# Optimization experiments

Measured on AMD Instinct MI355X. Metric: run time of the kernel, lower is better.

## Reference

```python
import jax, jax.numpy as jnp
import numpy as np

N, E = 100000, 1600000
IN, H, Z, C = 64, 128, 64, 2


def _glorot(key, fan_in, fan_out):
    s = jnp.sqrt(2.0 / (fan_in + fan_out)).astype(jnp.float32)
    return jax.random.normal(key, (fan_in, fan_out), dtype=jnp.float32) * s


def setup_inputs() -> dict:
    key = jax.random.key(0)
    ks = jax.random.split(key, 16)
    dims = [(IN, H), (H, H), (H, Z), (H, H), (H, Z), (Z, H), (H, H), (H, IN * C)]
    names = ['in', 'mu0', 'mu', 'si0', 'si', 'z', 'd0', 'out']
    inp = {
        'x': jax.random.normal(ks[0], (N, IN), dtype=jnp.float32),
        'eps': jax.random.normal(ks[1], (N, Z), dtype=jnp.float32),
        'edge_index': jax.random.randint(ks[2], (2, E), 0, N, dtype=jnp.int64),
    }
    for i, (nm, (fi, fo)) in enumerate(zip(names, dims)):
        inp[f'w_{nm}'] = _glorot(ks[3 + i], fi, fo)
        inp[f'b_{nm}'] = jnp.zeros((fo,), dtype=jnp.float32)
    return inp


def _gcn(x, W, b, src, dst, dinv):
    # PyG GCNConv: symmetric normalization with self-loops.
    h = x @ W                                      # [N, d_out]
    norm = (dinv[src] * dinv[dst])[:, None]        # [E, 1]
    agg = jax.ops.segment_sum(h[src] * norm, dst, num_segments=N)
    agg = agg + h * (dinv * dinv)[:, None]         # self-loop term (norm = 1/deg)
    return agg + b


def reference(x, edge_index, eps,
              w_in, b_in, w_mu0, b_mu0, w_mu, b_mu,
              w_si0, b_si0, w_si, b_si,
              w_z, b_z, w_d0, b_d0, w_out, b_out):
    src, dst = edge_index[0], edge_index[1]
    deg = jax.ops.segment_sum(jnp.ones((E,), jnp.float32), dst, num_segments=N) + 1.0
    dinv = jax.lax.rsqrt(deg)
    # encode
    h = jax.nn.relu(_gcn(x, w_in, b_in, src, dst, dinv))
    mu = jax.nn.relu(_gcn(h, w_mu0, b_mu0, src, dst, dinv))
    mu = jax.nn.relu(_gcn(mu, w_mu, b_mu, src, dst, dinv))
    si = jax.nn.relu(_gcn(h, w_si0, b_si0, src, dst, dinv))
    si = jax.nn.sigmoid(_gcn(si, w_si, b_si, src, dst, dinv))
    # reparameterize
    z = mu + si * eps
    # decode (first decoder layer has no activation, per the original forward)
    r = _gcn(z, w_z, b_z, src, dst, dinv)
    r = jax.nn.relu(_gcn(r, w_d0, b_d0, src, dst, dinv))
    logits = _gcn(r, w_out, b_out, src, dst, dinv)   # [N, IN*C]
    logits = logits.reshape(-1, C)                   # [N*IN, C]
    return logits, mu, si
```

## Files before the change

### kernel.cpp

```cpp
#include <hip/hip_runtime.h>


typedef short bf16x8 __attribute__((ext_vector_type(8)));
typedef float f32x4 __attribute__((ext_vector_type(4)));

__device__ __forceinline__ ushort f2bf(float f) {
    uint x = __float_as_uint(f);
    uint r = x + 0x7FFFu + ((x >> 16) & 1u);
    return (ushort)(r >> 16);
}
__device__ __forceinline__ float bf2f(ushort h) {
    return __uint_as_float(((uint)h) << 16);
}
__device__ __forceinline__ float dot2bf(uint a, uint b, float c) {
    float d;
    asm("v_dot2_f32_bf16 %0, %1, %2, %3" : "=v"(d) : "v"(a), "v"(b), "v"(c));
    return d;
}

__global__ __launch_bounds__(1024) void counts_kernel(const int* __restrict__ dst,
        int* __restrict__ deg, int* __restrict__ bc0, int E, int NB, int shift) {
    __shared__ int h[8192];
    for (int j = threadIdx.x; j < NB; j += 1024) h[j] = 0;
    __syncthreads();
    int stride = gridDim.x * 1024;
    for (int i = blockIdx.x * 1024 + threadIdx.x; i < E; i += stride) {
        int d = dst[i];
        atomicAdd(&deg[d], 1);
        atomicAdd(&h[d >> shift], 1);
    }
    __syncthreads();
    for (int j = threadIdx.x; j < NB; j += 1024) {
        int v = h[j];
        if (v) atomicAdd(&bc0[j], v);
    }
}

__global__ void dinv_kernel(const int* __restrict__ deg, float* __restrict__ dinv, int N) {
    int i = blockIdx.x * blockDim.x + threadIdx.x;
    if (i < N) dinv[i] = rsqrtf((float)(deg[i] + 1));
}

__global__ __launch_bounds__(1024) void scan_block_kernel(const int* __restrict__ in,
                                                          int* __restrict__ out,
                                                          int* __restrict__ bsum, int n) {
    __shared__ int s[1024];
    int i = blockIdx.x * 1024 + threadIdx.x;
    int v = (i < n) ? in[i] : 0;
    s[threadIdx.x] = v;
    __syncthreads();
    for (int off = 1; off < 1024; off <<= 1) {
        int t = (threadIdx.x >= off) ? s[threadIdx.x - off] : 0;
        __syncthreads();
        s[threadIdx.x] += t;
        __syncthreads();
    }
    if (i < n) out[i] = s[threadIdx.x] - v;
    if (threadIdx.x == 1023) bsum[blockIdx.x] = s[1023];
}

__global__ __launch_bounds__(1024) void scan_partials_kernel(int* __restrict__ bsum, int nb) {
    __shared__ int s[1024];
    int v = (threadIdx.x < nb) ? bsum[threadIdx.x] : 0;
    s[threadIdx.x] = v;
    __syncthreads();
    for (int off = 1; off < 1024; off <<= 1) {
        int t = (threadIdx.x >= off) ? s[threadIdx.x - off] : 0;
        __syncthreads();
        s[threadIdx.x] += t;
        __syncthreads();
    }
    if (threadIdx.x < nb) bsum[threadIdx.x] = s[threadIdx.x] - v;
}

__global__ __launch_bounds__(1024) void scan_add_kernel(int* __restrict__ arr,
                                                        const int* __restrict__ bsum, int n, int total) {
    int i = blockIdx.x * 1024 + threadIdx.x;
    if (i < n) arr[i] += bsum[blockIdx.x];
    if (i == 0) arr[n] = total;
}

__global__ void scatter_kernel(const int* __restrict__ src, const int* __restrict__ dst,
                               const int* __restrict__ bin_start, int* __restrict__ bc1,
                               int2* __restrict__ ebuf, int E, int shift) {
    int i = blockIdx.x * blockDim.x + threadIdx.x;
    if (i < E) {
        int d = dst[i];
        int b = d >> shift;
        int pos = bin_start[b] + atomicAdd(&bc1[b], 1);
        ebuf[pos] = make_int2(src[i], d);
    }
}

__global__ void place2_kernel(const int2* __restrict__ ebuf, const int* __restrict__ row_start,
                              int* __restrict__ cnt, int2* __restrict__ csr,
                              const float* __restrict__ dinv, int E) {
    int i = blockIdx.x * blockDim.x + threadIdx.x;
    if (i < E) {
        int2 e = ebuf[i];
        int pos = row_start[e.y] + atomicAdd(&cnt[e.y], 1);
        csr[pos] = make_int2(e.x, (int)(uint)f2bf(dinv[e.x] * dinv[e.y]));
    }
}

__global__ void rowsum_kernel(const int2* __restrict__ csr, const int* __restrict__ row_start,
                              const float* __restrict__ dinv, float* __restrict__ cvec, int N) {
    int j = blockIdx.x * blockDim.x + threadIdx.x;
    if (j >= N) return;
    float s = dinv[j] * dinv[j];
    int b = row_start[j], e = row_start[j + 1];
    for (int k = b; k < e; ++k) s += bf2f((ushort)((uint)csr[k].y & 0xFFFFu));
    cvec[j] = s;
}

__global__ void wcpack_kernel(const float* __restrict__ w_z, const float* __restrict__ b_z,
                              const float* __restrict__ w_d0,
                              ushort* __restrict__ P_wc, float* __restrict__ bzw) {
    int o = blockIdx.x * 256 + threadIdx.x;
    if (o >= 65 * 128) return;
    int i = o >> 7, j = o & 127;
    float s = 0.f;
    for (int k = 0; k < 128; ++k) {
        float a = (i < 64) ? w_z[i * 128 + k] : b_z[k];
        s = fmaf(a, w_d0[k * 128 + j], s);
    }
    if (i < 64) {
        int c = j >> 4, kb = i >> 5, l = ((i >> 3) & 3) * 16 + (j & 15), e = i & 7;
        P_wc[(size_t)((c * 2 + kb) * 64 + l) * 8 + e] = f2bf(s);
    } else bzw[j] = s;
}

__device__ __forceinline__ void pack_one(const float* __restrict__ W, ushort* __restrict__ P,
                                         int KI, int KO, int idx) {
    if (idx >= KI * KO) return;
    int e = idx & 7, l = (idx >> 3) & 63, t = idx >> 9;
    int KB = KI / 32;
    int c = t / KB, kb = t % KB;
    int k = kb * 32 + ((l >> 4) << 3) + e, col = c * 16 + (l & 15);
    P[idx] = f2bf(W[(size_t)k * KO + col]);
}

__global__ void megapack_kernel(const float* w_in, const float* w_mu0, const float* w_si0,
                                const float* w_mu, const float* w_si, const float* w_out,
                                ushort* P_in, ushort* P_mu0, ushort* P_si0,
                                ushort* P_mu, ushort* P_si, ushort* P_out) {
    int b = blockIdx.x, tid = threadIdx.x;
    if (b < 32)       pack_one(w_in,  P_in,  64, 128,  (b - 0)   * 256 + tid);
    else if (b < 96)  pack_one(w_mu0, P_mu0, 128, 128, (b - 32)  * 256 + tid);
    else if (b < 160) pack_one(w_si0, P_si0, 128, 128, (b - 96)  * 256 + tid);
    else if (b < 192) pack_one(w_mu,  P_mu,  128, 64,  (b - 160) * 256 + tid);
    else if (b < 224) pack_one(w_si,  P_si,  128, 64,  (b - 192) * 256 + tid);
    else              pack_one(w_out, P_out, 128, 128, (b - 224) * 256 + tid);
}

__global__ void cvt8_kernel(const float* __restrict__ in, ushort* __restrict__ out, int n8) {
    int i = blockIdx.x * 256 + threadIdx.x;
    if (i >= n8) return;
    float4 a = ((const float4*)in)[i * 2];
    float4 b = ((const float4*)in)[i * 2 + 1];
    bf16x8 o;
    o[0] = (short)f2bf(a.x); o[1] = (short)f2bf(a.y);
    o[2] = (short)f2bf(a.z); o[3] = (short)f2bf(a.w);
    o[4] = (short)f2bf(b.x); o[5] = (short)f2bf(b.y);
    o[6] = (short)f2bf(b.z); o[7] = (short)f2bf(b.w);
    ((bf16x8*)out)[i] = o;
}

template <int W, int DEPTH>
__device__ __forceinline__ void gather_pairs(float* acc, const ushort* __restrict__ xb,
        const int2* __restrict__ csr, int node, int beg, int end, int sub, int f8) {
    constexpr int SLOTS = 64 / (W / 8);
    for (int base = beg; base < end; base += 2 * SLOTS * DEPTH) {
        int sidx[DEPTH][2];
        uint wv[DEPTH][2];
        #pragma unroll
        for (int d = 0; d < DEPTH; ++d) {
            int e0 = base + 2 * (sub + SLOTS * d), e1 = e0 + 1;
            int2 p0 = csr[e0 < end ? e0 : beg];
            int2 p1 = csr[e1 < end ? e1 : beg];
            sidx[d][0] = (e0 < end) ? p0.x : node;
            sidx[d][1] = (e1 < end) ? p1.x : node;
            wv[d][0] = (e0 < end) ? (uint)p0.y : 0u;
            wv[d][1] = (e1 < end) ? (uint)p1.y : 0u;
        }
        uint4 rv[DEPTH][2];
        #pragma unroll
        for (int d = 0; d < DEPTH; ++d) {
            rv[d][0] = *(const uint4*)(xb + (size_t)sidx[d][0] * W + f8 * 8);
            rv[d][1] = *(const uint4*)(xb + (size_t)sidx[d][1] * W + f8 * 8);
        }
        #pragma unroll
        for (int d = 0; d < DEPTH; ++d) {
            uint wpk = __builtin_amdgcn_perm(wv[d][1], wv[d][0], 0x05040100u);
            uint4 v0 = rv[d][0], v1 = rv[d][1];
            uint t;
            t = __builtin_amdgcn_perm(v1.x, v0.x, 0x05040100u); acc[0] = dot2bf(t, wpk, acc[0]);
            t = __builtin_amdgcn_perm(v1.x, v0.x, 0x07060302u); acc[1] = dot2bf(t, wpk, acc[1]);
            t = __builtin_amdgcn_perm(v1.y, v0.y, 0x05040100u); acc[2] = dot2bf(t, wpk, acc[2]);
            t = __builtin_amdgcn_perm(v1.y, v0.y, 0x07060302u); acc[3] = dot2bf(t, wpk, acc[3]);
            t = __builtin_amdgcn_perm(v1.z, v0.z, 0x05040100u); acc[4] = dot2bf(t, wpk, acc[4]);
            t = __builtin_amdgcn_perm(v1.z, v0.z, 0x07060302u); acc[5] = dot2bf(t, wpk, acc[5]);
            t = __builtin_amdgcn_perm(v1.w, v0.w, 0x05040100u); acc[6] = dot2bf(t, wpk, acc[6]);
            t = __builtin_amdgcn_perm(v1.w, v0.w, 0x07060302u); acc[7] = dot2bf(t, wpk, acc[7]);
        }
    }
}

template <int W, int DEPTH>
__global__ __launch_bounds__(256) void bprop_kernel(const ushort* __restrict__ xb,
        ushort* __restrict__ out, const int* __restrict__ row_start,
        const int2* __restrict__ csr, const float* __restrict__ dinv, int N) {
    constexpr int L = W / 8;
    int wave = threadIdx.x >> 6, lane = threadIdx.x & 63;
    int node = blockIdx.x * 4 + wave;
    if (node >= N) return;
    int sub = lane / L, f8 = lane % L;
    int beg = row_start[node], end = row_start[node + 1];
    float d2 = dinv[node]; d2 *= d2;
    float acc[8] = {};
    gather_pairs<W, DEPTH>(acc, xb, csr, node, beg, end, sub, f8);
    #pragma unroll
    for (int m = L; m < 64; m <<= 1) {
        #pragma unroll
        for (int q = 0; q < 8; ++q) acc[q] += __shfl_xor(acc[q], m);
    }
    if (sub != 0) return;
    bf16x8 sv = *(const bf16x8*)(xb + (size_t)node * W + f8 * 8);
    bf16x8 oz;
    #pragma unroll
    for (int q = 0; q < 8; ++q) oz[q] = (short)f2bf(fmaf(d2, bf2f((ushort)sv[q]), acc[q]));
    *(bf16x8*)(out + (size_t)node * W + f8 * 8) = oz;
}

__global__ __launch_bounds__(256) void mssz_kernel(const ushort* __restrict__ T,
        const int* __restrict__ row_start, const int2* __restrict__ csr,
        const float* __restrict__ dinv, const float* __restrict__ b_mu,
        const float* __restrict__ b_si, const float* __restrict__ eps,
        float* __restrict__ M, float* __restrict__ S, ushort* __restrict__ zb, int N) {
    constexpr int L = 16;
    int wave = threadIdx.x >> 6, lane = threadIdx.x & 63;
    int node = blockIdx.x * 4 + wave;
    if (node >= N) return;
    int sub = lane / L, f8 = lane % L;
    int beg = row_start[node], end = row_start[node + 1];
    float d2 = dinv[node]; d2 *= d2;
    float acc[8] = {};
    gather_pairs<128, 2>(acc, T, csr, node, beg, end, sub, f8);
    #pragma unroll
    for (int m = 16; m < 64; m <<= 1) {
        #pragma unroll
        for (int q = 0; q < 8; ++q) acc[q] += __shfl_xor(acc[q], m);
    }
    if (sub != 0) return;
    bf16x8 sv = *(const bf16x8*)(T + (size_t)node * 128 + f8 * 8);
    #pragma unroll
    for (int q = 0; q < 8; ++q) acc[q] = fmaf(d2, bf2f((ushort)sv[q]), acc[q]);

    bool is_mu = (f8 < 8);
    const float* bp = is_mu ? b_mu : b_si;
    int o = (f8 & 7) * 8;
    float val[8];
    #pragma unroll
    for (int q = 0; q < 8; ++q) {
        float t = acc[q] + bp[o + q];
        val[q] = is_mu ? fmaxf(t, 0.f) : 1.f / (1.f + __expf(-t));
    }
    if (is_mu) {
        *(float4*)&M[(size_t)node * 64 + o]     = make_float4(val[0], val[1], val[2], val[3]);
        *(float4*)&M[(size_t)node * 64 + o + 4] = make_float4(val[4], val[5], val[6], val[7]);
    } else {
        *(float4*)&S[(size_t)node * 64 + o]     = make_float4(val[0], val[1], val[2], val[3]);
        *(float4*)&S[(size_t)node * 64 + o + 4] = make_float4(val[4], val[5], val[6], val[7]);
    }
    float oth[8];
    #pragma unroll
    for (int q = 0; q < 8; ++q) oth[q] = __shfl_xor(val[q], 8);
    if (is_mu) {
        float4 e0v = *(const float4*)&eps[(size_t)node * 64 + o];
        float4 e1v = *(const float4*)&eps[(size_t)node * 64 + o + 4];
        float ev[8] = {e0v.x, e0v.y, e0v.z, e0v.w, e1v.x, e1v.y, e1v.z, e1v.w};
        bf16x8 z;
        #pragma unroll
        for (int q = 0; q < 8; ++q) z[q] = (short)f2bf(fmaf(oth[q], ev[q], val[q]));
        *(bf16x8*)(zb + (size_t)node * 64 + o) = z;
    }
}

__global__ __launch_bounds__(256) void encgemm_kernel(const ushort* __restrict__ PH,
        const bf16x8* __restrict__ Pmu0, const float* __restrict__ b_mu0,
        const bf16x8* __restrict__ Pmu,
        const bf16x8* __restrict__ Psi0, const float* __restrict__ b_si0,
        const bf16x8* __restrict__ Psi,
        ushort* __restrict__ T, int N) {
    constexpr int STR = 136;
    __shared__ __align__(16) ushort Ls[64 * STR];
    int w = threadIdx.x >> 6, l = threadIdx.x & 63;
    int lr = l & 15, lk = l >> 4;
    int rowbase = blockIdx.x * 64;
    int arow = rowbase + w * 16 + lr; if (arow > N - 1) arow = N - 1;

    bf16x8 aph[4];
    const ushort* pp = PH + (size_t)arow * 128 + lk * 8;
    #pragma unroll
    for (int kb = 0; kb < 4; ++kb) aph[kb] = *(const bf16x8*)(pp + kb * 32);

    int crow0 = w * 16 + lk * 4;
    int afrow = w * 16 + lr;

    #pragma unroll
    for (int c = 0; c < 8; ++c) {
        f32x4 acc = {0.f, 0.f, 0.f, 0.f};
        #pragma unroll
        for (int kb = 0; kb < 4; ++kb)
            acc = __builtin_amdgcn_mfma_f32_16x16x32_bf16(aph[kb], Pmu0[((size_t)c * 4 + kb) * 64 + l], acc, 0, 0, 0);
        float bv = b_mu0[c * 16 + lr];
        #pragma unroll
        for (int r = 0; r < 4; ++r)
            Ls[(crow0 + r) * STR + c * 16 + lr] = f2bf(fmaxf(acc[r] + bv, 0.f));
    }
    __syncthreads();
    bf16x8 am[4];
    #pragma unroll
    for (int kb = 0; kb < 4; ++kb) am[kb] = *(const bf16x8*)&Ls[afrow * STR + kb * 32 + lk * 8];
    f32x4 tmu[4];
    #pragma unroll
    for (int c = 0; c < 4; ++c) {
        f32x4 acc = {0.f, 0.f, 0.f, 0.f};
        #pragma unroll
        for (int kb = 0; kb < 4; ++kb)
            acc = __builtin_amdgcn_mfma_f32_16x16x32_bf16(am[kb], Pmu[((size_t)c * 4 + kb) * 64 + l], acc, 0, 0, 0);
        tmu[c] = acc;
    }
    __syncthreads();
    #pragma unroll
    for (int c = 0; c < 8; ++c) {
        f32x4 acc = {0.f, 0.f, 0.f, 0.f};
        #pragma unroll
        for (int kb = 0; kb < 4; ++kb)
            acc = __builtin_amdgcn_mfma_f32_16x16x32_bf16(aph[kb], Psi0[((size_t)c * 4 + kb) * 64 + l], acc, 0, 0, 0);
        float bv = b_si0[c * 16 + lr];
        #pragma unroll
        for (int r = 0; r < 4; ++r)
            Ls[(crow0 + r) * STR + c * 16 + lr] = f2bf(fmaxf(acc[r] + bv, 0.f));
    }
    __syncthreads();
    #pragma unroll
    for (int kb = 0; kb < 4; ++kb) am[kb] = *(const bf16x8*)&Ls[afrow * STR + kb * 32 + lk * 8];
    f32x4 tsi[4];
    #pragma unroll
    for (int c = 0; c < 4; ++c) {
        f32x4 acc = {0.f, 0.f, 0.f, 0.f};
        #pragma unroll
        for (int kb = 0; kb < 4; ++kb)
            acc = __builtin_amdgcn_mfma_f32_16x16x32_bf16(am[kb], Psi[((size_t)c * 4 + kb) * 64 + l], acc, 0, 0, 0);
        tsi[c] = acc;
    }
    __syncthreads();
    #pragma unroll
    for (int c = 0; c < 4; ++c) {
        #pragma unroll
        for (int r = 0; r < 4; ++r) {
            Ls[(crow0 + r) * STR + c * 16 + lr]      = f2bf(tmu[c][r]);
            Ls[(crow0 + r) * STR + 64 + c * 16 + lr] = f2bf(tsi[c][r]);
        }
    }
    __syncthreads();
    for (int idx = threadIdx.x; idx < 64 * 16; idx += 256) {
        int row = idx >> 4, c8 = idx & 15;
        if (rowbase + row < N) {
            bf16x8 vv = *(const bf16x8*)&Ls[row * STR + c8 * 8];
            *(bf16x8*)(T + (size_t)(rowbase + row) * 128 + c8 * 8) = vv;
        }
    }
}

template <int KI, int KO, int EPI, int OUT>
__global__ __launch_bounds__(256) void mgemm_kernel(const ushort* __restrict__ Xb,
                                                    const bf16x8* __restrict__ Wp,
                                                    const float* __restrict__ bias,
                                                    const float* __restrict__ bias2,
                                                    const float* __restrict__ cvec,
                                                    void* __restrict__ outp, int ostride, int N) {
    constexpr int KB = KI / 32;
    constexpr int CT = KO / 16;
    constexpr size_t LSB = (OUT == 1) ? (size_t)64 * KO * 4 : (size_t)64 * KO * 2;
    __shared__ __align__(16) char LsRaw[LSB];

    int w = threadIdx.x >> 6, l = threadIdx.x & 63;
    int lr = l & 15, lk = l >> 4;
    int rowbase = blockIdx.x * 64;
    int r0 = rowbase + w * 16;

    int arow = r0 + lr; if (arow > N - 1) arow = N - 1;
    bf16x8 a[KB];
    const ushort* xp = Xb + (size_t)arow * KI + lk * 8;
    #pragma unroll
    for (int kb = 0; kb < KB; ++kb) a[kb] = *(const bf16x8*)(xp + kb * 32);

    float cv[4];
    if constexpr (EPI == 3) {
        #pragma unroll
        for (int r = 0; r < 4; ++r) {
            int rr = r0 + lk * 4 + r;
            cv[r] = cvec[rr < N ? rr : 0];
        }
    }

    #pragma unroll
    for (int c = 0; c < CT; ++c) {
        f32x4 acc = {0.f, 0.f, 0.f, 0.f};
        #pragma unroll
        for (int kb = 0; kb < KB; ++kb)
            acc = __builtin_amdgcn_mfma_f32_16x16x32_bf16(a[kb], Wp[((size_t)c * KB + kb) * 64 + l], acc, 0, 0, 0);
        int col = c * 16 + lr;
        float bv = 0.f, b2v = 0.f;
        if constexpr (EPI >= 1) bv = bias[col];
        if constexpr (EPI == 3) b2v = bias2[col];
        #pragma unroll
        for (int r = 0; r < 4; ++r) {
            float v = acc[r];
            if constexpr (EPI == 1) v += bv;
            if constexpr (EPI == 2) v = fmaxf(v + bv, 0.f);
            if constexpr (EPI == 3) v = fmaxf(v + cv[r] * bv + b2v, 0.f);
            int rl = w * 16 + lk * 4 + r;
            if constexpr (OUT == 0) ((ushort*)LsRaw)[(size_t)rl * KO + col] = f2bf(v);
            else                    ((float*)LsRaw)[(size_t)rl * KO + col] = v;
        }
    }
    __syncthreads();

    if constexpr (OUT == 0) {
        ushort* o = (ushort*)outp;
        constexpr int CH = 64 * KO / 8;
        for (int idx = threadIdx.x; idx < CH; idx += 256) {
            int row = idx / (KO / 8), c8 = idx % (KO / 8);
            if (rowbase + row < N)
                *(bf16x8*)(o + (size_t)(rowbase + row) * ostride + c8 * 8) = ((const bf16x8*)LsRaw)[idx];
        }
    } else {
        float* o = (float*)outp;
        constexpr int CH = 64 * KO / 4;
        for (int idx = threadIdx.x; idx < CH; idx += 256) {
            int row = idx / (KO / 4), c4 = idx % (KO / 4);
            if (rowbase + row < N)
                *(float4*)(o + (size_t)(rowbase + row) * ostride + c4 * 4) = ((const float4*)LsRaw)[idx];
        }
    }
}

extern "C" void kernel_launch(void* const* d_in, const int* in_sizes, int n_in,
                              void* d_out, int out_size, void* d_ws, size_t ws_size,
                              hipStream_t stream) {
    const float* x    = (const float*)d_in[0];
    const float* eps  = (const float*)d_in[1];
    const int*   ei   = (const int*)d_in[2];
    const float* w_in  = (const float*)d_in[3];  const float* b_in  = (const float*)d_in[4];
    const float* w_mu0 = (const float*)d_in[5];  const float* b_mu0 = (const float*)d_in[6];
    const float* w_mu  = (const float*)d_in[7];  const float* b_mu  = (const float*)d_in[8];
    const float* w_si0 = (const float*)d_in[9];  const float* b_si0 = (const float*)d_in[10];
    const float* w_si  = (const float*)d_in[11]; const float* b_si  = (const float*)d_in[12];
    const float* w_z   = (const float*)d_in[13]; const float* b_z   = (const float*)d_in[14];
    const float* w_d0  = (const float*)d_in[15]; const float* b_d0  = (const float*)d_in[16];
    const float* w_out = (const float*)d_in[17]; const float* b_out = (const float*)d_in[18];

    const int N = in_sizes[0] / 64;
    const int E = in_sizes[2] / 2;
    const int* srcI = ei;
    const int* dstI = ei + E;

    int shift = 4;
    while (((N >> shift) + 1) > 8192) shift++;
    const int NB = (N >> shift) + 1;

    auto align = [](size_t v) { return (v + 255) & ~(size_t)255; };
    char* wsp = (char*)d_ws;
    size_t off = 0;
    int*    deg       = (int*)(wsp + off);    size_t deg_off = off; off = align(off + (size_t)N * 4);
    int*    bc0       = (int*)(wsp + off);    off = align(off + (size_t)NB * 4);
    int*    bc1       = (int*)(wsp + off);    off = align(off + (size_t)NB * 4);
    size_t  zero_span = off - deg_off;
    float*  cvec      = (float*)(wsp + off);  off = align(off + (size_t)N * 4);
    int*    row_start = (int*)(wsp + off);    off = align(off + (size_t)(N + 1) * 4);
    int*    bin_start = (int*)(wsp + off);    off = align(off + (size_t)(NB + 1) * 4);
    int*    bsum      = (int*)(wsp + off);    off = align(off + 1024 * 4);
    float*  dinv      = (float*)(wsp + off);  off = align(off + (size_t)N * 4);
    float*  bzw       = (float*)(wsp + off);  off = align(off + 128 * 4);
    ushort* P_in      = (ushort*)(wsp + off); off = align(off + 64 * 128 * 2);
    ushort* P_mu0     = (ushort*)(wsp + off); off = align(off + 128 * 128 * 2);
    ushort* P_si0     = (ushort*)(wsp + off); off = align(off + 128 * 128 * 2);
    ushort* P_mu      = (ushort*)(wsp + off); off = align(off + 128 * 64 * 2);
    ushort* P_si      = (ushort*)(wsp + off); off = align(off + 128 * 64 * 2);
    ushort* P_wc      = (ushort*)(wsp + off); off = align(off + 64 * 128 * 2);
    ushort* P_out     = (ushort*)(wsp + off); off = align(off + 128 * 128 * 2);
    int2*   csr       = (int2*)(wsp + off);   off = align(off + (size_t)E * 8);
    int2*   ebuf      = (int2*)(wsp + off);   off = align(off + (size_t)E * 8);
    ushort* xb        = (ushort*)ebuf;
    ushort* B1        = (ushort*)(wsp + off); off = align(off + (size_t)N * 128 * 2);
    ushort* B1lo = B1;
    ushort* B1hi = B1 + (size_t)N * 64;

    float* Cc = (float*)d_out;
    float* M  = Cc + (size_t)N * 128;
    float* S  = M + (size_t)N * 64;
    ushort* CcLo = (ushort*)Cc;
    ushort* CcHi = (ushort*)(Cc + (size_t)N * 64);
    ushort* Db   = (ushort*)M;

    const int TB = 256;
    hipMemsetAsync(deg, 0, zero_span, stream);
    counts_kernel<<<256, 1024, 0, stream>>>(dstI, deg, bc0, E, NB, shift);
    dinv_kernel<<<(N + TB - 1) / TB, TB, 0, stream>>>(deg, dinv, N);
    int nbN = (N + 1023) / 1024;
    scan_block_kernel<<<nbN, 1024, 0, stream>>>(deg, row_start, bsum, N);
    scan_partials_kernel<<<1, 1024, 0, stream>>>(bsum, nbN);
    scan_add_kernel<<<nbN, 1024, 0, stream>>>(row_start, bsum, N, E);
    int nbB = (NB + 1023) / 1024;
    scan_block_kernel<<<nbB, 1024, 0, stream>>>(bc0, bin_start, bsum, NB);
    scan_partials_kernel<<<1, 1024, 0, stream>>>(bsum, nbB);
    scan_add_kernel<<<nbB, 1024, 0, stream>>>(bin_start, bsum, NB, E);
    hipMemsetAsync(deg, 0, (size_t)N * 4, stream);
    scatter_kernel<<<(E + TB - 1) / TB, TB, 0, stream>>>(srcI, dstI, bin_start, bc1, ebuf, E, shift);
    place2_kernel<<<(E + TB - 1) / TB, TB, 0, stream>>>(ebuf, row_start, deg, csr, dinv, E);
    rowsum_kernel<<<(N + TB - 1) / TB, TB, 0, stream>>>(csr, row_start, dinv, cvec, N);
    wcpack_kernel<<<(65 * 128 + 255) / 256, 256, 0, stream>>>(w_z, b_z, w_d0, P_wc, bzw);
    megapack_kernel<<<288, 256, 0, stream>>>(w_in, w_mu0, w_si0, w_mu, w_si, w_out,
                                             P_in, P_mu0, P_si0, P_mu, P_si, P_out);
    cvt8_kernel<<<((N * 8) + 255) / 256, 256, 0, stream>>>(x, xb, N * 8);

    int PG = (N + 3) / 4;
    int GB = (N + 63) / 64;

    bprop_kernel<64, 1><<<PG, 256, 0, stream>>>(xb, B1lo, row_start, csr, dinv, N);
    mgemm_kernel<64, 128, 2, 0><<<GB, 256, 0, stream>>>(B1lo, (const bf16x8*)P_in, b_in, nullptr, nullptr, CcLo, 128, N);
    bprop_kernel<128, 2><<<PG, 256, 0, stream>>>(CcLo, Db, row_start, csr, dinv, N);
    encgemm_kernel<<<GB, 256, 0, stream>>>(Db,
                                           (const bf16x8*)P_mu0, b_mu0, (const bf16x8*)P_mu,
                                           (const bf16x8*)P_si0, b_si0, (const bf16x8*)P_si,
                                           CcHi, N);
    mssz_kernel<<<PG, 256, 0, stream>>>(CcHi, row_start, csr, dinv, b_mu, b_si, eps, M, S, B1lo, N);
    bprop_kernel<64, 1><<<PG, 256, 0, stream>>>(B1lo, B1hi, row_start, csr, dinv, N);
    bprop_kernel<64, 1><<<PG, 256, 0, stream>>>(B1hi, xb, row_start, csr, dinv, N);
    mgemm_kernel<64, 128, 3, 0><<<GB, 256, 0, stream>>>(xb, (const bf16x8*)P_wc, bzw, b_d0, cvec, CcLo, 128, N);
    bprop_kernel<128, 2><<<PG, 256, 0, stream>>>(CcLo, B1, row_start, csr, dinv, N);
    mgemm_kernel<128, 128, 1, 1><<<GB, 256, 0, stream>>>(B1, (const bf16x8*)P_out, b_out, nullptr, nullptr, Cc, 128, N);
}
```

Baseline: 660.1 us.

## Process two nodes per wave in SpMM propagation with software-pipelined gathers

After: 654.3 us. Within noise of the previous version (-0.9%).

```diff
diff --git a/kernel.cpp b/kernel.cpp
--- a/kernel.cpp
+++ b/kernel.cpp
@@ -166,96 +166,137 @@
     ((bf16x8*)out)[i] = o;
 }
 
-template <int W, int DEPTH>
-__device__ __forceinline__ void gather_pairs(float* acc, const ushort* __restrict__ xb,
-        const int2* __restrict__ csr, int node, int beg, int end, int sub, int f8) {
-    constexpr int SLOTS = 64 / (W / 8);
-    for (int base = beg; base < end; base += 2 * SLOTS * DEPTH) {
-        int sidx[DEPTH][2];
-        uint wv[DEPTH][2];
-        #pragma unroll
-        for (int d = 0; d < DEPTH; ++d) {
-            int e0 = base + 2 * (sub + SLOTS * d), e1 = e0 + 1;
-            int2 p0 = csr[e0 < end ? e0 : beg];
-            int2 p1 = csr[e1 < end ? e1 : beg];
-            sidx[d][0] = (e0 < end) ? p0.x : node;
-            sidx[d][1] = (e1 < end) ? p1.x : node;
-            wv[d][0] = (e0 < end) ? (uint)p0.y : 0u;
-            wv[d][1] = (e1 < end) ? (uint)p1.y : 0u;
-        }
-        uint4 rv[DEPTH][2];
-        #pragma unroll
-        for (int d = 0; d < DEPTH; ++d) {
-            rv[d][0] = *(const uint4*)(xb + (size_t)sidx[d][0] * W + f8 * 8);
-            rv[d][1] = *(const uint4*)(xb + (size_t)sidx[d][1] * W + f8 * 8);
-        }
-        #pragma unroll
-        for (int d = 0; d < DEPTH; ++d) {
-            uint wpk = __builtin_amdgcn_perm(wv[d][1], wv[d][0], 0x05040100u);
-            uint4 v0 = rv[d][0], v1 = rv[d][1];
-            uint t;
-            t = __builtin_amdgcn_perm(v1.x, v0.x, 0x05040100u); acc[0] = dot2bf(t, wpk, acc[0]);
-            t = __builtin_amdgcn_perm(v1.x, v0.x, 0x07060302u); acc[1] = dot2bf(t, wpk, acc[1]);
-            t = __builtin_amdgcn_perm(v1.y, v0.y, 0x05040100u); acc[2] = dot2bf(t, wpk, acc[2]);
-            t = __builtin_amdgcn_perm(v1.y, v0.y, 0x07060302u); acc[3] = dot2bf(t, wpk, acc[3]);
-            t = __builtin_amdgcn_perm(v1.z, v0.z, 0x05040100u); acc[4] = dot2bf(t, wpk, acc[4]);
-            t = __builtin_amdgcn_perm(v1.z, v0.z, 0x07060302u); acc[5] = dot2bf(t, wpk, acc[5]);
-            t = __builtin_amdgcn_perm(v1.w, v0.w, 0x05040100u); acc[6] = dot2bf(t, wpk, acc[6]);
-            t = __builtin_amdgcn_perm(v1.w, v0.w, 0x07060302u); acc[7] = dot2bf(t, wpk, acc[7]);
-        }
-    }
-}
-
-template <int W, int DEPTH>
-__global__ __launch_bounds__(256) void bprop_kernel(const ushort* __restrict__ xb,
+template <int W>
+struct GS {
+    static constexpr int L = W / 8;
+    static constexpr int SLOTS = 64 / L;
+    static constexpr int PP = 16 / (2 * SLOTS);
+    int2 c[2 * PP];
+    uint4 r[2 * PP];
+};
+
+template <int W>
+__device__ __forceinline__ void g_csr(GS<W>& st, const int2* __restrict__ csr,
+                                      int base, int beg, int end, int sub) {
+    int safe = (end > beg) ? beg : 0;
+    #pragma unroll
+    for (int p = 0; p < GS<W>::PP; ++p) {
+        int e0 = base + 2 * (sub + GS<W>::SLOTS * p);
+        st.c[2 * p]     = csr[e0 < end ? e0 : safe];
+        st.c[2 * p + 1] = csr[e0 + 1 < end ? e0 + 1 : safe];
+    }
+}
+
+template <int W>
+__device__ __forceinline__ void g_rows(GS<W>& st, const ushort* __restrict__ xb, int f8) {
+    #pragma unroll
+    for (int i = 0; i < 2 * GS<W>::PP; ++i)
+        st.r[i] = *(const uint4*)(xb + (size_t)st.c[i].x * W + f8 * 8);
+}
+
+template <int W>
+__device__ __forceinline__ void g_consume(GS<W>& st, float* acc, int base, int end, int sub) {
+    #pragma unroll
+    for (int p = 0; p < GS<W>::PP; ++p) {
+        int e0 = base + 2 * (sub + GS<W>::SLOTS * p);
+        uint w0 = (e0 < end) ? (uint)st.c[2 * p].y : 0u;
+        uint w1 = (e0 + 1 < end) ? (uint)st.c[2 * p + 1].y : 0u;
+        uint wpk = __builtin_amdgcn_perm(w1, w0, 0x05040100u);
+        uint4 v0 = st.r[2 * p], v1 = st.r[2 * p + 1];
+        uint t;
+        t = __builtin_amdgcn_perm(v1.x, v0.x, 0x05040100u); acc[0] = dot2bf(t, wpk, acc[0]);
+        t = __builtin_amdgcn_perm(v1.x, v0.x, 0x07060302u); acc[1] = dot2bf(t, wpk, acc[1]);
+        t = __builtin_amdgcn_perm(v1.y, v0.y, 0x05040100u); acc[2] = dot2bf(t, wpk, acc[2]);
+        t = __builtin_amdgcn_perm(v1.y, v0.y, 0x07060302u); acc[3] = dot2bf(t, wpk, acc[3]);
+        t = __builtin_amdgcn_perm(v1.z, v0.z, 0x05040100u); acc[4] = dot2bf(t, wpk, acc[4]);
+        t = __builtin_amdgcn_perm(v1.z, v0.z, 0x07060302u); acc[5] = dot2bf(t, wpk, acc[5]);
+        t = __builtin_amdgcn_perm(v1.w, v0.w, 0x05040100u); acc[6] = dot2bf(t, wpk, acc[6]);
+        t = __builtin_amdgcn_perm(v1.w, v0.w, 0x07060302u); acc[7] = dot2bf(t, wpk, acc[7]);
+    }
+}
+
+template <int W>
+__global__ __launch_bounds__(256) void pprop_kernel(const ushort* __restrict__ xb,
         ushort* __restrict__ out, const int* __restrict__ row_start,
         const int2* __restrict__ csr, const float* __restrict__ dinv, int N) {
     constexpr int L = W / 8;
     int wave = threadIdx.x >> 6, lane = threadIdx.x & 63;
-    int node = blockIdx.x * 4 + wave;
-    if (node >= N) return;
+    int nb = (blockIdx.x * 4 + wave) * 2;
+    if (nb >= N) return;
     int sub = lane / L, f8 = lane % L;
-    int beg = row_start[node], end = row_start[node + 1];
-    float d2 = dinv[node]; d2 *= d2;
-    float acc[8] = {};
-    gather_pairs<W, DEPTH>(acc, xb, csr, node, beg, end, sub, f8);
+    bool v1 = (nb + 1) < N;
+    int n0 = nb, n1 = v1 ? nb + 1 : nb;
+
+    int2 rs01 = *(const int2*)&row_start[nb];
+    int rs2 = row_start[v1 ? nb + 2 : nb + 1];
+    int beg0 = rs01.x, end0 = rs01.y;
+    int beg1 = rs01.y, end1 = v1 ? rs2 : rs01.y;
+
+    float d20 = dinv[n0], d21 = dinv[n1];
+    bf16x8 sv0 = *(const bf16x8*)(xb + (size_t)n0 * W + f8 * 8);
+    bf16x8 sv1 = *(const bf16x8*)(xb + (size_t)n1 * W + f8 * 8);
+
+    GS<W> sA, sB, sA2, sB2;
+    g_csr(sA, csr, beg0, beg0, end0, sub);
+    g_csr(sB, csr, beg1, beg1, end1, sub);
+    g_csr(sA2, csr, beg0 + 16, beg0, end0, sub);
+    g_csr(sB2, csr, beg1 + 16, beg1, end1, sub);
+    g_rows(sA, xb, f8);
+    g_rows(sB, xb, f8);
+
+    float a0[8] = {}, a1[8] = {};
+    bool m0 = (beg0 + 16) < end0, m1 = (beg1 + 16) < end1;
+    g_consume(sA, a0, beg0, end0, sub);
+    if (m0) g_rows(sA2, xb, f8);
+    g_consume(sB, a1, beg1, end1, sub);
+    if (m1) g_rows(sB2, xb, f8);
+    if (m0) {
+        g_consume(sA2, a0, beg0 + 16, end0, sub);
+        for (int base = beg0 + 32; base < end0; base += 16) {
+            GS<W> t;
+            g_csr(t, csr, base, beg0, end0, sub);
+            g_rows(t, xb, f8);
+            g_consume(t, a0, base, end0, sub);
+        }
+    }
+    if (m1) {
+        g_consume(sB2, a1, beg1 + 16, end1, sub);
+        for (int base = beg1 + 32; base < end1; base += 16) {
+            GS<W> t;
+            g_csr(t, csr, base, beg1, end1, sub);
+            g_rows(t, xb, f8);
+            g_consume(t, a1, base, end1, sub);
+        }
+    }
+
     #pragma unroll
     for (int m = L; m < 64; m <<= 1) {
         #pragma unroll
-        for (int q = 0; q < 8; ++q) acc[q] += __shfl_xor(acc[q], m);
-    }
-    if (sub != 0) return;
-    bf16x8 sv = *(const bf16x8*)(xb + (size_t)node * W + f8 * 8);
-    bf16x8 oz;
-    #pragma unroll
-    for (int q = 0; q < 8; ++q) oz[q] = (short)f2bf(fmaf(d2, bf2f((ushort)sv[q]), acc[q]));
-    *(bf16x8*)(out + (size_t)node * W + f8 * 8) = oz;
-}
-
-__global__ __launch_bounds__(256) void mssz_kernel(const ushort* __restrict__ T,
-        const int* __restrict__ row_start, const int2* __restrict__ csr,
-        const float* __restrict__ dinv, const float* __restrict__ b_mu,
-        const float* __restrict__ b_si, const float* __restrict__ eps,
-        float* __restrict__ M, float* __restrict__ S, ushort* __restrict__ zb, int N) {
-    constexpr int L = 16;
-    int wave = threadIdx.x >> 6, lane = threadIdx.x & 63;
-    int node = blockIdx.x * 4 + wave;
-    if (node >= N) return;
-    int sub = lane / L, f8 = lane % L;
-    int beg = row_start[node], end = row_start[node + 1];
-    float d2 = dinv[node]; d2 *= d2;
-    float acc[8] = {};
-    gather_pairs<128, 2>(acc, T, csr, node, beg, end, sub, f8);
-    #pragma unroll
-    for (int m = 16; m < 64; m <<= 1) {
-        #pragma unroll
-        for (int q = 0; q < 8; ++q) acc[q] += __shfl_xor(acc[q], m);
-    }
-    if (sub != 0) return;
-    bf16x8 sv = *(const bf16x8*)(T + (size_t)node * 128 + f8 * 8);
-    #pragma unroll
-    for (int q = 0; q < 8; ++q) acc[q] = fmaf(d2, bf2f((ushort)sv[q]), acc[q]);
-
+        for (int q = 0; q < 8; ++q) {
+            a0[q] += __shfl_xor(a0[q], m);
+            a1[q] += __shfl_xor(a1[q], m);
+        }
+    }
+    if (sub == 0) {
+        float d2 = d20 * d20;
+        bf16x8 o0;
+        #pragma unroll
+        for (int q = 0; q < 8; ++q) o0[q] = (short)f2bf(fmaf(d2, bf2f((ushort)sv0[q]), a0[q]));
+        *(bf16x8*)(out + (size_t)n0 * W + f8 * 8) = o0;
+        if (v1) {
+            float e2 = d21 * d21;
+            bf16x8 o1;
+            #pragma unroll
+            for (int q = 0; q < 8; ++q) o1[q] = (short)f2bf(fmaf(e2, bf2f((ushort)sv1[q]), a1[q]));
+            *(bf16x8*)(out + (size_t)n1 * W + f8 * 8) = o1;
+        }
+    }
+}
+
+__device__ __forceinline__ void mssz_epi(const float* acc, int node, int f8,
+        const float* __restrict__ b_mu, const float* __restrict__ b_si,
+        const float* __restrict__ eps, float* __restrict__ M, float* __restrict__ S,
+        ushort* __restrict__ zb) {
     bool is_mu = (f8 < 8);
     const float* bp = is_mu ? b_mu : b_si;
     int o = (f8 & 7) * 8;
@@ -283,6 +324,83 @@
         #pragma unroll
         for (int q = 0; q < 8; ++q) z[q] = (short)f2bf(fmaf(oth[q], ev[q], val[q]));
         *(bf16x8*)(zb + (size_t)node * 64 + o) = z;
+    }
+}
+
+__global__ __launch_bounds__(256) void pmssz_kernel(const ushort* __restrict__ T,
+        const int* __restrict__ row_start, const int2* __restrict__ csr,
+        const float* __restrict__ dinv, const float* __restrict__ b_mu,
+        const float* __restrict__ b_si, const float* __restrict__ eps,
+        float* __restrict__ M, float* __restrict__ S, ushort* __restrict__ zb, int N) {
+    constexpr int W = 128, L = 16;
+    int wave = threadIdx.x >> 6, lane = threadIdx.x & 63;
+    int nb = (blockIdx.x * 4 + wave) * 2;
+    if (nb >= N) return;
+    int sub = lane / L, f8 = lane % L;
+    bool v1 = (nb + 1) < N;
+    int n0 = nb, n1 = v1 ? nb + 1 : nb;
+
+    int2 rs01 = *(const int2*)&row_start[nb];
+    int rs2 = row_start[v1 ? nb + 2 : nb + 1];
+    int beg0 = rs01.x, end0 = rs01.y;
+    int beg1 = rs01.y, end1 = v1 ? rs2 : rs01.y;
+
+    float d20 = dinv[n0], d21 = dinv[n1];
+    bf16x8 sv0 = *(const bf16x8*)(T + (size_t)n0 * W + f8 * 8);
+    bf16x8 sv1 = *(const bf16x8*)(T + (size_t)n1 * W + f8 * 8);
+
+    GS<W> sA, sB, sA2, sB2;
+    g_csr(sA, csr, beg0, beg0, end0, sub);
+    g_csr(sB, csr, beg1, beg1, end1, sub);
+    g_csr(sA2, csr, beg0 + 16, beg0, end0, sub);
+    g_csr(sB2, csr, beg1 + 16, beg1, end1, sub);
+    g_rows(sA, T, f8);
+    g_rows(sB, T, f8);
+
+    float a0[8] = {}, a1[8] = {};
+    bool m0 = (beg0 + 16) < end0, m1 = (beg1 + 16) < end1;
+    g_consume(sA, a0, beg0, end0, sub);
+    if (m0) g_rows(sA2, T, f8);
+    g_consume(sB, a1, beg1, end1, sub);
+    if (m1) g_rows(sB2, T, f8);
+    if (m0) {
+        g_consume(sA2, a0, beg0 + 16, end0, sub);
+        for (int base = beg0 + 32; base < end0; base += 16) {
+            GS<W> t;
+            g_csr(t, csr, base, beg0, end0, sub);
+            g_rows(t, T, f8);
+            g_consume(t, a0, base, end0, sub);
+        }
+    }
+    if (m1) {
+        g_consume(sB2, a1, beg1 + 16, end1, sub);
+        for (int base = beg1 + 32; base < end1; base += 16) {
+            GS<W> t;
+            g_csr(t, csr, base, beg1, end1, sub);
+            g_rows(t, T, f8);
+            g_consume(t, a1, base, end1, sub);
+        }
+    }
+
+    #pragma unroll
+    for (int m = L; m < 64; m <<= 1) {
+        #pragma unroll
+        for (int q = 0; q < 8; ++q) {
+            a0[q] += __shfl_xor(a0[q], m);
+            a1[q] += __shfl_xor(a1[q], m);
+        }
+    }
+    if (sub == 0) {
+        float d2 = d20 * d20;
+        #pragma unroll
+        for (int q = 0; q < 8; ++q) a0[q] = fmaf(d2, bf2f((ushort)sv0[q]), a0[q]);
+        mssz_epi(a0, n0, f8, b_mu, b_si, eps, M, S, zb);
+        if (v1) {
+            float e2 = d21 * d21;
+            #pragma unroll
+            for (int q = 0; q < 8; ++q) a1[q] = fmaf(e2, bf2f((ushort)sv1[q]), a1[q]);
+            mssz_epi(a1, n1, f8, b_mu, b_si, eps, M, S, zb);
+        }
     }
 }
 
@@ -527,20 +645,20 @@
                                              P_in, P_mu0, P_si0, P_mu, P_si, P_out);
     cvt8_kernel<<<((N * 8) + 255) / 256, 256, 0, stream>>>(x, xb, N * 8);
 
-    int PG = (N + 3) / 4;
+    int PG = (N + 7) / 8;
     int GB = (N + 63) / 64;
 
-    bprop_kernel<64, 1><<<PG, 256, 0, stream>>>(xb, B1lo, row_start, csr, dinv, N);
+    pprop_kernel<64><<<PG, 256, 0, stream>>>(xb, B1lo, row_start, csr, dinv, N);
     mgemm_kernel<64, 128, 2, 0><<<GB, 256, 0, stream>>>(B1lo, (const bf16x8*)P_in, b_in, nullptr, nullptr, CcLo, 128, N);
-    bprop_kernel<128, 2><<<PG, 256, 0, stream>>>(CcLo, Db, row_start, csr, dinv, N);
+    pprop_kernel<128><<<PG, 256, 0, stream>>>(CcLo, Db, row_start, csr, dinv, N);
     encgemm_kernel<<<GB, 256, 0, stream>>>(Db,
                                            (const bf16x8*)P_mu0, b_mu0, (const bf16x8*)P_mu,
                                            (const bf16x8*)P_si0, b_si0, (const bf16x8*)P_si,
                                            CcHi, N);
-    mssz_kernel<<<PG, 256, 0, stream>>>(CcHi, row_start, csr, dinv, b_mu, b_si, eps, M, S, B1lo, N);
-    bprop_kernel<64, 1><<<PG, 256, 0, stream>>>(B1lo, B1hi, row_start, csr, dinv, N);
-    bprop_kernel<64, 1><<<PG, 256, 0, stream>>>(B1hi, xb, row_start, csr, dinv, N);
+    pmssz_kernel<<<PG, 256, 0, stream>>>(CcHi, row_start, csr, dinv, b_mu, b_si, eps, M, S, B1lo, N);
+    pprop_kernel<64><<<PG, 256, 0, stream>>>(B1lo, B1hi, row_start, csr, dinv, N);
+    pprop_kernel<64><<<PG, 256, 0, stream>>>(B1hi, xb, row_start, csr, dinv, N);
     mgemm_kernel<64, 128, 3, 0><<<GB, 256, 0, stream>>>(xb, (const bf16x8*)P_wc, bzw, b_d0, cvec, CcLo, 128, N);
-    bprop_kernel<128, 2><<<PG, 256, 0, stream>>>(CcLo, B1, row_start, csr, dinv, N);
+    pprop_kernel<128><<<PG, 256, 0, stream>>>(CcLo, B1, row_start, csr, dinv, N);
     mgemm_kernel<128, 128, 1, 1><<<GB, 256, 0, stream>>>(B1, (const bf16x8*)P_out, b_out, nullptr, nullptr, Cc, 128, N);
 }
```

## Pack CSR entries into 32-bit words and feature-slice sparse propagation across blocks

Applied to the files above, without the earlier changes.

Measured after the change: 1.553 ms. 135% more time.

```diff
diff --git a/kernel.cpp b/kernel.cpp
--- a/kernel.cpp
+++ b/kernel.cpp
@@ -12,10 +12,15 @@
 __device__ __forceinline__ float bf2f(ushort h) {
     return __uint_as_float(((uint)h) << 16);
 }
-__device__ __forceinline__ float dot2bf(uint a, uint b, float c) {
-    float d;
-    asm("v_dot2_f32_bf16 %0, %1, %2, %3" : "=v"(d) : "v"(a), "v"(b), "v"(c));
-    return d;
+__device__ __forceinline__ void fma8(float* acc, uint4 v, float w) {
+    acc[0] = fmaf(w, __uint_as_float(v.x << 16), acc[0]);
+    acc[1] = fmaf(w, __uint_as_float(v.x & 0xFFFF0000u), acc[1]);
+    acc[2] = fmaf(w, __uint_as_float(v.y << 16), acc[2]);
+    acc[3] = fmaf(w, __uint_as_float(v.y & 0xFFFF0000u), acc[3]);
+    acc[4] = fmaf(w, __uint_as_float(v.z << 16), acc[4]);
+    acc[5] = fmaf(w, __uint_as_float(v.z & 0xFFFF0000u), acc[5]);
+    acc[6] = fmaf(w, __uint_as_float(v.w << 16), acc[6]);
+    acc[7] = fmaf(w, __uint_as_float(v.w & 0xFFFF0000u), acc[7]);
 }
 
 __global__ __launch_bounds__(1024) void counts_kernel(const int* __restrict__ dst,
@@ -93,23 +98,24 @@
 }
 
 __global__ void place2_kernel(const int2* __restrict__ ebuf, const int* __restrict__ row_start,
-                              int* __restrict__ cnt, int2* __restrict__ csr,
+                              int* __restrict__ cnt, uint* __restrict__ csrp,
                               const float* __restrict__ dinv, int E) {
     int i = blockIdx.x * blockDim.x + threadIdx.x;
     if (i < E) {
         int2 e = ebuf[i];
         int pos = row_start[e.y] + atomicAdd(&cnt[e.y], 1);
-        csr[pos] = make_int2(e.x, (int)(uint)f2bf(dinv[e.x] * dinv[e.y]));
-    }
-}
-
-__global__ void rowsum_kernel(const int2* __restrict__ csr, const int* __restrict__ row_start,
+        uint wb = (uint)f2bf(dinv[e.x] * dinv[e.y]) & 0x7FFFu;
+        csrp[pos] = ((uint)e.x << 15) | wb;
+    }
+}
+
+__global__ void rowsum_kernel(const uint* __restrict__ csrp, const int* __restrict__ row_start,
                               const float* __restrict__ dinv, float* __restrict__ cvec, int N) {
     int j = blockIdx.x * blockDim.x + threadIdx.x;
     if (j >= N) return;
     float s = dinv[j] * dinv[j];
     int b = row_start[j], e = row_start[j + 1];
-    for (int k = b; k < e; ++k) s += bf2f((ushort)((uint)csr[k].y & 0xFFFFu));
+    for (int k = b; k < e; ++k) s += __uint_as_float((csrp[k] & 0x7FFFu) << 16);
     cvec[j] = s;
 }
 
@@ -166,116 +172,126 @@
     ((bf16x8*)out)[i] = o;
 }
 
-template <int W, int DEPTH>
-__device__ __forceinline__ void gather_pairs(float* acc, const ushort* __restrict__ xb,
-        const int2* __restrict__ csr, int node, int beg, int end, int sub, int f8) {
-    constexpr int SLOTS = 64 / (W / 8);
-    for (int base = beg; base < end; base += 2 * SLOTS * DEPTH) {
-        int sidx[DEPTH][2];
-        uint wv[DEPTH][2];
-        #pragma unroll
-        for (int d = 0; d < DEPTH; ++d) {
-            int e0 = base + 2 * (sub + SLOTS * d), e1 = e0 + 1;
-            int2 p0 = csr[e0 < end ? e0 : beg];
-            int2 p1 = csr[e1 < end ? e1 : beg];
-            sidx[d][0] = (e0 < end) ? p0.x : node;
-            sidx[d][1] = (e1 < end) ? p1.x : node;
-            wv[d][0] = (e0 < end) ? (uint)p0.y : 0u;
-            wv[d][1] = (e1 < end) ? (uint)p1.y : 0u;
-        }
-        uint4 rv[DEPTH][2];
-        #pragma unroll
-        for (int d = 0; d < DEPTH; ++d) {
-            rv[d][0] = *(const uint4*)(xb + (size_t)sidx[d][0] * W + f8 * 8);
-            rv[d][1] = *(const uint4*)(xb + (size_t)sidx[d][1] * W + f8 * 8);
-        }
-        #pragma unroll
-        for (int d = 0; d < DEPTH; ++d) {
-            uint wpk = __builtin_amdgcn_perm(wv[d][1], wv[d][0], 0x05040100u);
-            uint4 v0 = rv[d][0], v1 = rv[d][1];
-            uint t;
-            t = __builtin_amdgcn_perm(v1.x, v0.x, 0x05040100u); acc[0] = dot2bf(t, wpk, acc[0]);
-            t = __builtin_amdgcn_perm(v1.x, v0.x, 0x07060302u); acc[1] = dot2bf(t, wpk, acc[1]);
-            t = __builtin_amdgcn_perm(v1.y, v0.y, 0x05040100u); acc[2] = dot2bf(t, wpk, acc[2]);
-            t = __builtin_amdgcn_perm(v1.y, v0.y, 0x07060302u); acc[3] = dot2bf(t, wpk, acc[3]);
-            t = __builtin_amdgcn_perm(v1.z, v0.z, 0x05040100u); acc[4] = dot2bf(t, wpk, acc[4]);
-            t = __builtin_amdgcn_perm(v1.z, v0.z, 0x07060302u); acc[5] = dot2bf(t, wpk, acc[5]);
-            t = __builtin_amdgcn_perm(v1.w, v0.w, 0x05040100u); acc[6] = dot2bf(t, wpk, acc[6]);
-            t = __builtin_amdgcn_perm(v1.w, v0.w, 0x07060302u); acc[7] = dot2bf(t, wpk, acc[7]);
-        }
-    }
-}
-
-template <int W, int DEPTH>
-__global__ __launch_bounds__(256) void bprop_kernel(const ushort* __restrict__ xb,
+
+__global__ __launch_bounds__(256) void sprop64_kernel(const ushort* __restrict__ xb,
         ushort* __restrict__ out, const int* __restrict__ row_start,
-        const int2* __restrict__ csr, const float* __restrict__ dinv, int N) {
-    constexpr int L = W / 8;
+        const uint* __restrict__ csrp, const float* __restrict__ dinv, int N) {
+    int b = blockIdx.x;
+    int fs = b & 7, chunk = b >> 3;
     int wave = threadIdx.x >> 6, lane = threadIdx.x & 63;
-    int node = blockIdx.x * 4 + wave;
+    int grp = lane >> 4, slot = lane & 15;
+    int node = chunk * 16 + wave * 4 + grp;
     if (node >= N) return;
-    int sub = lane / L, f8 = lane % L;
     int beg = row_start[node], end = row_start[node + 1];
+    const ushort* base_x = xb + (size_t)fs * 8;
+
+    float acc[8] = {};
+    for (int base = beg; base < end; base += 16) {
+        int e = base + slot;
+        bool v = e < end;
+        uint ent = csrp[v ? e : 0];
+        float w = v ? __uint_as_float((ent & 0x7FFFu) << 16) : 0.f;
+        uint4 r = *(const uint4*)(base_x + (size_t)(ent >> 15) * 64);
+        fma8(acc, r, w);
+    }
+    #pragma unroll
+    for (int m = 1; m < 16; m <<= 1) {
+        #pragma unroll
+        for (int q = 0; q < 8; ++q) acc[q] += __shfl_xor(acc[q], m);
+    }
+    if (slot != 0) return;
     float d2 = dinv[node]; d2 *= d2;
+    uint4 sv = *(const uint4*)(base_x + (size_t)node * 64);
+    fma8(acc, sv, d2);
+    bf16x8 o;
+    #pragma unroll
+    for (int q = 0; q < 8; ++q) o[q] = (short)f2bf(acc[q]);
+    *(bf16x8*)(out + (size_t)node * 64 + fs * 8) = o;
+}
+
+__global__ __launch_bounds__(256) void sprop128_kernel(const ushort* __restrict__ xb,
+        ushort* __restrict__ out, const int* __restrict__ row_start,
+        const uint* __restrict__ csrp, const float* __restrict__ dinv, int N) {
+    int b = blockIdx.x;
+    int fs = b & 7, chunk = b >> 3;
+    int wave = threadIdx.x >> 6, lane = threadIdx.x & 63;
+    int grp = lane >> 5, slot = (lane >> 1) & 15, p = lane & 1;
+    int node = chunk * 8 + wave * 2 + grp;
+    if (node >= N) return;
+    int beg = row_start[node], end = row_start[node + 1];
+    const ushort* base_x = xb + (size_t)fs * 16 + p * 8;
+
     float acc[8] = {};
-    gather_pairs<W, DEPTH>(acc, xb, csr, node, beg, end, sub, f8);
-    #pragma unroll
-    for (int m = L; m < 64; m <<= 1) {
+    for (int base = beg; base < end; base += 16) {
+        int e = base + slot;
+        bool v = e < end;
+        uint ent = csrp[v ? e : 0];
+        float w = v ? __uint_as_float((ent & 0x7FFFu) << 16) : 0.f;
+        uint4 r = *(const uint4*)(base_x + (size_t)(ent >> 15) * 128);
+        fma8(acc, r, w);
+    }
+    #pragma unroll
+    for (int m = 2; m < 32; m <<= 1) {
         #pragma unroll
         for (int q = 0; q < 8; ++q) acc[q] += __shfl_xor(acc[q], m);
     }
-    if (sub != 0) return;
-    bf16x8 sv = *(const bf16x8*)(xb + (size_t)node * W + f8 * 8);
-    bf16x8 oz;
-    #pragma unroll
-    for (int q = 0; q < 8; ++q) oz[q] = (short)f2bf(fmaf(d2, bf2f((ushort)sv[q]), acc[q]));
-    *(bf16x8*)(out + (size_t)node * W + f8 * 8) = oz;
-}
-
-__global__ __launch_bounds__(256) void mssz_kernel(const ushort* __restrict__ T,
-        const int* __restrict__ row_start, const int2* __restrict__ csr,
+    if (slot != 0) return;
+    float d2 = dinv[node]; d2 *= d2;
+    uint4 sv = *(const uint4*)(base_x + (size_t)node * 128);
+    fma8(acc, sv, d2);
+    bf16x8 o;
+    #pragma unroll
+    for (int q = 0; q < 8; ++q) o[q] = (short)f2bf(acc[q]);
+    *(bf16x8*)(out + (size_t)node * 128 + fs * 16 + p * 8) = o;
+}
+
+__global__ __launch_bounds__(256) void smssz_kernel(const ushort* __restrict__ T,
+        const int* __restrict__ row_start, const uint* __restrict__ csrp,
         const float* __restrict__ dinv, const float* __restrict__ b_mu,
         const float* __restrict__ b_si, const float* __restrict__ eps,
         float* __restrict__ M, float* __restrict__ S, ushort* __restrict__ zb, int N) {
-    constexpr int L = 16;
+    int b = blockIdx.x;
+    int fs = b & 7, chunk = b >> 3;
     int wave = threadIdx.x >> 6, lane = threadIdx.x & 63;
-    int node = blockIdx.x * 4 + wave;
+    int grp = lane >> 5, slot = (lane >> 1) & 15, p = lane & 1;
+    int node = chunk * 8 + wave * 2 + grp;
     if (node >= N) return;
-    int sub = lane / L, f8 = lane % L;
     int beg = row_start[node], end = row_start[node + 1];
+    const ushort* base_x = T + (size_t)fs * 16 + p * 8;
+
+    float acc[8] = {};
+    for (int base = beg; base < end; base += 16) {
+        int e = base + slot;
+        bool v = e < end;
+        uint ent = csrp[v ? e : 0];
+        float w = v ? __uint_as_float((ent & 0x7FFFu) << 16) : 0.f;
+        uint4 r = *(const uint4*)(base_x + (size_t)(ent >> 15) * 128);
+        fma8(acc, r, w);
+    }
+    #pragma unroll
+    for (int m = 2; m < 32; m <<= 1) {
+        #pragma unroll
+        for (int q = 0; q < 8; ++q) acc[q] += __shfl_xor(acc[q], m);
+    }
     float d2 = dinv[node]; d2 *= d2;
-    float acc[8] = {};
-    gather_pairs<128, 2>(acc, T, csr, node, beg, end, sub, f8);
-    #pragma unroll
-    for (int m = 16; m < 64; m <<= 1) {
-        #pragma unroll
-        for (int q = 0; q < 8; ++q) acc[q] += __shfl_xor(acc[q], m);
-    }
-    if (sub != 0) return;
-    bf16x8 sv = *(const bf16x8*)(T + (size_t)node * 128 + f8 * 8);
-    #pragma unroll
-    for (int q = 0; q < 8; ++q) acc[q] = fmaf(d2, bf2f((ushort)sv[q]), acc[q]);
-
-    bool is_mu = (f8 < 8);
-    const float* bp = is_mu ? b_mu : b_si;
-    int o = (f8 & 7) * 8;
+    uint4 sv = *(const uint4*)(base_x + (size_t)node * 128);
+    fma8(acc, sv, d2);
+
+    const float* bp = (p == 0) ? b_mu : b_si;
+    int o = fs * 8;
     float val[8];
     #pragma unroll
     for (int q = 0; q < 8; ++q) {
         float t = acc[q] + bp[o + q];
-        val[q] = is_mu ? fmaxf(t, 0.f) : 1.f / (1.f + __expf(-t));
-    }
-    if (is_mu) {
+        val[q] = (p == 0) ? fmaxf(t, 0.f) : 1.f / (1.f + __expf(-t));
+    }
+    float oth[8];
+    #pragma unroll
+    for (int q = 0; q < 8; ++q) oth[q] = __shfl_xor(val[q], 1);
+    if (slot != 0) return;
+    if (p == 0) {
         *(float4*)&M[(size_t)node * 64 + o]     = make_float4(val[0], val[1], val[2], val[3]);
         *(float4*)&M[(size_t)node * 64 + o + 4] = make_float4(val[4], val[5], val[6], val[7]);
-    } else {
-        *(float4*)&S[(size_t)node * 64 + o]     = make_float4(val[0], val[1], val[2], val[3]);
-        *(float4*)&S[(size_t)node * 64 + o + 4] = make_float4(val[4], val[5], val[6], val[7]);
-    }
-    float oth[8];
-    #pragma unroll
-    for (int q = 0; q < 8; ++q) oth[q] = __shfl_xor(val[q], 8);
-    if (is_mu) {
         float4 e0v = *(const float4*)&eps[(size_t)node * 64 + o];
         float4 e1v = *(const float4*)&eps[(size_t)node * 64 + o + 4];
         float ev[8] = {e0v.x, e0v.y, e0v.z, e0v.w, e1v.x, e1v.y, e1v.z, e1v.w};
@@ -283,6 +299,9 @@
         #pragma unroll
         for (int q = 0; q < 8; ++q) z[q] = (short)f2bf(fmaf(oth[q], ev[q], val[q]));
         *(bf16x8*)(zb + (size_t)node * 64 + o) = z;
+    } else {
+        *(float4*)&S[(size_t)node * 64 + o]     = make_float4(val[0], val[1], val[2], val[3]);
+        *(float4*)&S[(size_t)node * 64 + o + 4] = make_float4(val[4], val[5], val[6], val[7]);
     }
 }
 
@@ -356,12 +375,17 @@
         tsi[c] = acc;
     }
     __syncthreads();
+    {
+        int colm = ((lr >> 3) + 2 * 0) * 16;
+        (void)colm;
+    }
     #pragma unroll
     for (int c = 0; c < 4; ++c) {
+        int colm = c * 32 + (lr >> 3) * 16 + (lr & 7);
         #pragma unroll
         for (int r = 0; r < 4; ++r) {
-            Ls[(crow0 + r) * STR + c * 16 + lr]      = f2bf(tmu[c][r]);
-            Ls[(crow0 + r) * STR + 64 + c * 16 + lr] = f2bf(tsi[c][r]);
+            Ls[(crow0 + r) * STR + colm]     = f2bf(tmu[c][r]);
+            Ls[(crow0 + r) * STR + colm + 8] = f2bf(tsi[c][r]);
         }
     }
     __syncthreads();
@@ -492,7 +516,7 @@
     ushort* P_si      = (ushort*)(wsp + off); off = align(off + 128 * 64 * 2);
     ushort* P_wc      = (ushort*)(wsp + off); off = align(off + 64 * 128 * 2);
     ushort* P_out     = (ushort*)(wsp + off); off = align(off + 128 * 128 * 2);
-    int2*   csr       = (int2*)(wsp + off);   off = align(off + (size_t)E * 8);
+    uint*   csrp      = (uint*)(wsp + off);   off = align(off + (size_t)(E + 64) * 4);
     int2*   ebuf      = (int2*)(wsp + off);   off = align(off + (size_t)E * 8);
     ushort* xb        = (ushort*)ebuf;
     ushort* B1        = (ushort*)(wsp + off); off = align(off + (size_t)N * 128 * 2);
@@ -520,27 +544,28 @@
     scan_add_kernel<<<nbB, 1024, 0, stream>>>(bin_start, bsum, NB, E);
     hipMemsetAsync(deg, 0, (size_t)N * 4, stream);
     scatter_kernel<<<(E + TB - 1) / TB, TB, 0, stream>>>(srcI, dstI, bin_start, bc1, ebuf, E, shift);
-    place2_kernel<<<(E + TB - 1) / TB, TB, 0, stream>>>(ebuf, row_start, deg, csr, dinv, E);
-    rowsum_kernel<<<(N + TB - 1) / TB, TB, 0, stream>>>(csr, row_start, dinv, cvec, N);
+    place2_kernel<<<(E + TB - 1) / TB, TB, 0, stream>>>(ebuf, row_start, deg, csrp, dinv, E);
+    rowsum_kernel<<<(N + TB - 1) / TB, TB, 0, stream>>>(csrp, row_start, dinv, cvec, N);
     wcpack_kernel<<<(65 * 128 + 255) / 256, 256, 0, stream>>>(w_z, b_z, w_d0, P_wc, bzw);
     megapack_kernel<<<288, 256, 0, stream>>>(w_in, w_mu0, w_si0, w_mu, w_si, w_out,
                                              P_in, P_mu0, P_si0, P_mu, P_si, P_out);
     cvt8_kernel<<<((N * 8) + 255) / 256, 256, 0, stream>>>(x, xb, N * 8);
 
-    int PG = (N + 3) / 4;
+    int PG64  = 8 * ((N + 15) / 16);
+    int PG128 = 8 * ((N + 7) / 8);
     int GB = (N + 63) / 64;
 
-    bprop_kernel<64, 1><<<PG, 256, 0, stream>>>(xb, B1lo, row_start, csr, dinv, N);
+    sprop64_kernel<<<PG64, 256, 0, stream>>>(xb, B1lo, row_start, csrp, dinv, N);
     mgemm_kernel<64, 128, 2, 0><<<GB, 256, 0, stream>>>(B1lo, (const bf16x8*)P_in, b_in, nullptr, nullptr, CcLo, 128, N);
-    bprop_kernel<128, 2><<<PG, 256, 0, stream>>>(CcLo, Db, row_start, csr, dinv, N);
+    sprop128_kernel<<<PG128, 256, 0, stream>>>(CcLo, Db, row_start, csrp, dinv, N);
     encgemm_kernel<<<GB, 256, 0, stream>>>(Db,
                                            (const bf16x8*)P_mu0, b_mu0, (const bf16x8*)P_mu,
                                            (const bf16x8*)P_si0, b_si0, (const bf16x8*)P_si,
                                            CcHi, N);
-    mssz_kernel<<<PG, 256, 0, stream>>>(CcHi, row_start, csr, dinv, b_mu, b_si, eps, M, S, B1lo, N);
-    bprop_kernel<64, 1><<<PG, 256, 0, stream>>>(B1lo, B1hi, row_start, csr, dinv, N);
-    bprop_kernel<64, 1><<<PG, 256, 0, stream>>>(B1hi, xb, row_start, csr, dinv, N);
+    smssz_kernel<<<PG128, 256, 0, stream>>>(CcHi, row_start, csrp, dinv, b_mu, b_si, eps, M, S, B1lo, N);
+    sprop64_kernel<<<PG64, 256, 0, stream>>>(B1lo, B1hi, row_start, csrp, dinv, N);
+    sprop64_kernel<<<PG64, 256, 0, stream>>>(B1hi, xb, row_start, csrp, dinv, N);
     mgemm_kernel<64, 128, 3, 0><<<GB, 256, 0, stream>>>(xb, (const bf16x8*)P_wc, bzw, b_d0, cvec, CcLo, 128, N);
-    bprop_kernel<128, 2><<<PG, 256, 0, stream>>>(CcLo, B1, row_start, csr, dinv, N);
+    sprop128_kernel<<<PG128, 256, 0, stream>>>(CcLo, B1, row_start, csrp, dinv, N);
     mgemm_kernel<128, 128, 1, 1><<<GB, 256, 0, stream>>>(B1, (const bf16x8*)P_out, b_out, nullptr, nullptr, Cc, 128, N);
 }
```
